# Performance work log

Hardware: AMD Instinct MI355X
Metric: run time of the kernel (lower is better)

The kernel has to match this reference:

```python
import jax, jax.numpy as jnp
import numpy as np

DIM = 2048
H = 16
HD = DIM // H          # 128
ROPE_CH = (HD // 2) // 2 * 2  # 64
EPS = 1e-6
SCALE = HD ** -0.5
MAX_WAVELENGTH = 10000.0


def rmsnorm(v, w):
    vf = v.astype(jnp.float32)
    var = jnp.mean(vf * vf, axis=-1, keepdims=True)
    return (w * (vf * jax.lax.rsqrt(var + EPS))).astype(v.dtype)


def apply_rope(v, pos):
    # v: [B, S, H, C], pos: [B, S]
    C = v.shape[-1]
    frac = 2.0 * jnp.arange(C // 2, dtype=jnp.float32) / C
    timescale = MAX_WAVELENGTH ** frac                      # [C/2]
    ang = pos[:, :, None].astype(jnp.float32) / timescale   # [B, S, C/2]
    ang = ang[:, :, None, :]                                 # [B, S, 1, C/2]
    sin, cos = jnp.sin(ang), jnp.cos(ang)
    v1, v2 = jnp.split(v, 2, axis=-1)
    return jnp.concatenate([v1 * cos - v2 * sin, v2 * cos + v1 * sin], axis=-1).astype(v.dtype)


def apply_rotary_emb(v, pos, channels):
    # rope only the last `channels` of head_dim
    left, right = v[..., :-channels], v[..., -channels:]
    return jnp.concatenate([left, apply_rope(right, pos)], axis=-1)


def project_qkv(t, W, b, qn, kn):
    B, N, _ = t.shape
    qkv = t @ W + b                                          # [B, N, 3*H*HD]
    q, k, v = jnp.split(qkv, [H * HD, 2 * H * HD], axis=-1)
    q = rmsnorm(q.reshape(B, N, H, HD), qn)
    k = rmsnorm(k.reshape(B, N, H, HD), kn)
    v = v.reshape(B, N, H, HD)
    return q, k, v


def setup_inputs() -> dict:
    key = jax.random.key(0)
    ks = jax.random.split(key, 12)
    B, NX, NY = 2, 2048, 512
    x = jax.random.normal(ks[0], (B, NX, DIM), dtype=jnp.float32)
    y = jax.random.normal(ks[1], (B, NY, DIM), dtype=jnp.float32)
    temporal_pos = jax.random.randint(ks[2], (B, NX), 0, 2048)
    y_temporal_pos = jax.random.randint(ks[3], (B, NY), 0, 512)
    s = 0.02
    Wqkv_x = jax.random.normal(ks[4], (DIM, 3 * H * HD), dtype=jnp.float32) * s
    bqkv_x = jnp.zeros((3 * H * HD,), dtype=jnp.float32)
    Wqkv_y = jax.random.normal(ks[5], (DIM, 3 * H * HD), dtype=jnp.float32) * s
    bqkv_y = jnp.zeros((3 * H * HD,), dtype=jnp.float32)
    Wproj_x = jax.random.normal(ks[6], (DIM, DIM), dtype=jnp.float32) * s
    bproj_x = jnp.zeros((DIM,), dtype=jnp.float32)
    Wproj_y = jax.random.normal(ks[7], (DIM, DIM), dtype=jnp.float32) * s
    bproj_y = jnp.zeros((DIM,), dtype=jnp.float32)
    qnx = jnp.ones((HD,), dtype=jnp.float32)
    knx = jnp.ones((HD,), dtype=jnp.float32)
    qny = jnp.ones((HD,), dtype=jnp.float32)
    kny = jnp.ones((HD,), dtype=jnp.float32)
    return {"x": x, "y": y, "temporal_pos": temporal_pos, "y_temporal_pos": y_temporal_pos,
            "Wqkv_x": Wqkv_x, "bqkv_x": bqkv_x, "qnx": qnx, "knx": knx,
            "Wproj_x": Wproj_x, "bproj_x": bproj_x,
            "Wqkv_y": Wqkv_y, "bqkv_y": bqkv_y, "qny": qny, "kny": kny,
            "Wproj_y": Wproj_y, "bproj_y": bproj_y}


def reference(x, y, temporal_pos, y_temporal_pos,
              Wqkv_x, bqkv_x, qnx, knx, Wproj_x, bproj_x,
              Wqkv_y, bqkv_y, qny, kny, Wproj_y, bproj_y):
    B, NX, _ = x.shape
    NY = y.shape[1]
    qx, kx, vx = project_qkv(x, Wqkv_x, bqkv_x, qnx, knx)   # [B, NX, H, HD]
    qy, ky, vy = project_qkv(y, Wqkv_y, bqkv_y, qny, kny)   # [B, NY, H, HD]
    # RoPE on last ROPE_CH channels of head_dim (rope_dim=-1)
    qx = apply_rotary_emb(qx, temporal_pos, ROPE_CH)
    kx = apply_rotary_emb(kx, temporal_pos, ROPE_CH)
    qy = apply_rotary_emb(qy, y_temporal_pos, ROPE_CH)
    ky = apply_rotary_emb(ky, y_temporal_pos, ROPE_CH)
    # joint attention over concatenated x/y tokens
    q = jnp.concatenate([qx, qy], axis=1)   # [B, S, H, HD]
    k = jnp.concatenate([kx, ky], axis=1)
    v = jnp.concatenate([vx, vy], axis=1)
    scores = jnp.einsum('bqhd,bkhd->bhqk', q, k) * SCALE
    attn = jax.nn.softmax(scores, axis=-1)
    out = jnp.einsum('bhqk,bkhd->bqhd', attn, v)             # [B, S, H, HD]
    out = out.reshape(B, NX + NY, DIM).astype(x.dtype)
    x_out = out[:, :NX] @ Wproj_x + bproj_x
    y_out = out[:, NX:] @ Wproj_y + bproj_y
    return (x_out, y_out)
```

## Files before the change

### kernel.cpp

```cpp
#include <hip/hip_runtime.h>
#include <stdint.h>

typedef __attribute__((ext_vector_type(8))) short v8s;
typedef __attribute__((ext_vector_type(4))) float v4f;

#define DEV static __device__ __forceinline__

DEV unsigned short f2bf(float f) {
  union { float f; unsigned int u; } v; v.f = f;
  unsigned int u = v.u;
  return (unsigned short)((u + 0x7fffu + ((u >> 16) & 1u)) >> 16);
}

DEV v4f mfma16(v8s a, v8s b, v4f c) {
  return __builtin_amdgcn_mfma_f32_16x16x32_bf16(a, b, c, 0, 0, 0);
}

DEV unsigned int cvtpk(float lo, float hi) {
  unsigned int r;
  asm("v_cvt_pk_bf16_f32 %0, %1, %2" : "=v"(r) : "v"(lo), "v"(hi));
  return r;
}

DEV void async16(const void* g, void* lds) {
  __builtin_amdgcn_global_load_lds((const __attribute__((address_space(1))) unsigned int*)g,
                                   (__attribute__((address_space(3))) unsigned int*)lds,
                                   16, 0, 0);
}

__global__ __launch_bounds__(256) void k_f32_to_bf16(const float* __restrict__ in,
                                                     unsigned short* __restrict__ out, int n4) {
  int i = blockIdx.x * 256 + threadIdx.x;
  if (i < n4) {
    float4 v = reinterpret_cast<const float4*>(in)[i];
    ushort4 o;
    o.x = f2bf(v.x); o.y = f2bf(v.y); o.z = f2bf(v.z); o.w = f2bf(v.w);
    reinterpret_cast<ushort4*>(out)[i] = o;
  }
}

__global__ __launch_bounds__(256) void k_rope_tbl(const int* __restrict__ pos,
                                                  float* __restrict__ tbl, int nrows) {
  int idx = blockIdx.x * 256 + threadIdx.x;
  if (idx < nrows * 32) {
    int row = idx >> 5, i = idx & 31;
    float ang = (float)pos[row] * expf((float)i * -0.2878231366f);
    float sv, cv;
    sincosf(ang, &sv, &cv);
    reinterpret_cast<float2*>(tbl)[(size_t)row * 32 + i] = make_float2(cv, sv);
  }
}

__global__ __launch_bounds__(256) void k_transpose(const float* __restrict__ in,
                                                   unsigned short* __restrict__ out, int R, int C) {
  __shared__ float tile[64][65];
  const int r0 = blockIdx.x * 64, c0 = blockIdx.y * 64;
  const int t = threadIdx.x;
  const int rl = t >> 4, cl = (t & 15) * 4;
#pragma unroll
  for (int p = 0; p < 4; p++) {
    const int r = rl + p * 16;
    float4 v = *reinterpret_cast<const float4*>(&in[(size_t)(r0 + r) * C + c0 + cl]);
    tile[r][cl] = v.x; tile[r][cl + 1] = v.y; tile[r][cl + 2] = v.z; tile[r][cl + 3] = v.w;
  }
  __syncthreads();
  const int cw = t >> 4, rw = (t & 15) * 4;
#pragma unroll
  for (int p = 0; p < 4; p++) {
    const int c = cw + p * 16;
    ushort4 o;
    o.x = f2bf(tile[rw + 0][c]); o.y = f2bf(tile[rw + 1][c]);
    o.z = f2bf(tile[rw + 2][c]); o.w = f2bf(tile[rw + 3][c]);
    *reinterpret_cast<ushort4*>(&out[(size_t)(c0 + c) * R + r0 + rw]) = o;
  }
}

template <int MODE>
__global__ __launch_bounds__(256) void k_gemm(
    const unsigned short* __restrict__ A, const unsigned short* __restrict__ Bt,
    const float* __restrict__ bias, float* __restrict__ Cout,
    unsigned short* __restrict__ Qb, unsigned short* __restrict__ Kb,
    unsigned short* __restrict__ Vt, const float* __restrict__ qn,
    const float* __restrict__ kn, const float* __restrict__ rtbl, int K, int N, int Nm, int noff,
    int rows_per_b, int b_stride, int row_off) {
  __shared__ __align__(16) char Lds[3 * 16384];
  __shared__ float red[4][64];
  const int m0 = blockIdx.x * 128, n0 = blockIdx.y * 128;
  const int t = threadIdx.x, l = t & 63, w = t >> 6;
  const int lg = l >> 4, li = l & 15;
  const int sr = t >> 2, ss = t & 3;

  auto amap = [&](int m) -> size_t {
    return (size_t)(m / rows_per_b) * b_stride + row_off + (m % rows_per_b);
  };
  const int ssw = (ss ^ ((sr >> 1) & 3)) * 8;
  const unsigned short* ap0 = A + amap(m0 + sr) * K + ssw;
  const unsigned short* ap1 = A + amap(m0 + sr + 64) * K + ssw;
  const unsigned short* bp0 = Bt + (size_t)(n0 + sr) * K + ssw;
  const unsigned short* bp1 = bp0 + (size_t)64 * K;

  auto stage = [&](char* lb, int st) {
    const int ko = st * 32;
    async16(ap0 + ko, lb + w * 1024);
    async16(ap1 + ko, lb + w * 1024 + 4096);
    async16(bp0 + ko, lb + 8192 + w * 1024);
    async16(bp1 + ko, lb + 8192 + w * 1024 + 4096);
  };

  int aoff[4], boff[4];
#pragma unroll
  for (int mf = 0; mf < 4; mf++) {
    const int row = (w >> 1) * 64 + mf * 16 + li;
    aoff[mf] = row * 64 + ((lg ^ ((row >> 1) & 3)) * 16);
  }
#pragma unroll
  for (int nf = 0; nf < 4; nf++) {
    const int row = (w & 1) * 64 + nf * 16 + li;
    boff[nf] = 8192 + row * 64 + ((lg ^ ((row >> 1) & 3)) * 16);
  }

  v4f acc[4][4] = {};
  const int NK = K >> 5;

  stage(Lds, 0);
  stage(Lds + 16384, 1);
  stage(Lds + 32768, 2);

  int bufc = 0;
  for (int tt = 0; tt < NK; tt++) {
    asm volatile("s_waitcnt vmcnt(8)" ::: "memory");
    __builtin_amdgcn_sched_barrier(0);
    __builtin_amdgcn_s_barrier();
    __builtin_amdgcn_sched_barrier(0);
    char* Bf = Lds + bufc;
    v8s af[4], bf[4];
#pragma unroll
    for (int mf = 0; mf < 4; mf++) af[mf] = *reinterpret_cast<const v8s*>(Bf + aoff[mf]);
#pragma unroll
    for (int nf = 0; nf < 4; nf++) bf[nf] = *reinterpret_cast<const v8s*>(Bf + boff[nf]);
    __builtin_amdgcn_s_setprio(1);
#pragma unroll
    for (int mf = 0; mf < 4; mf++)
#pragma unroll
      for (int nf = 0; nf < 4; nf++)
        acc[mf][nf] = mfma16(af[mf], bf[nf], acc[mf][nf]);
    __builtin_amdgcn_s_setprio(0);
    __builtin_amdgcn_sched_barrier(0);
    __builtin_amdgcn_s_barrier();
    __builtin_amdgcn_sched_barrier(0);
    const int st = (tt + 3 < NK) ? tt + 3 : NK - 1;
    stage(Bf, st);
    bufc += 16384;
    if (bufc == 49152) bufc = 0;
  }
  asm volatile("s_waitcnt vmcnt(0)" ::: "memory");

  const int colh = (w & 1) * 64;
#pragma unroll
  for (int nf = 0; nf < 4; nf++) {
    const float bv = bias[n0 + colh + nf * 16 + li];
#pragma unroll
    for (int mf = 0; mf < 4; mf++)
#pragma unroll
      for (int r = 0; r < 4; r++) acc[mf][nf][r] += bv;
  }

  if (MODE == 0) {
#pragma unroll
    for (int mf = 0; mf < 4; mf++) {
      const int row = m0 + (w >> 1) * 64 + mf * 16 + lg * 4;
#pragma unroll
      for (int nf = 0; nf < 4; nf++) {
        const int col = n0 + colh + nf * 16 + li;
#pragma unroll
        for (int r = 0; r < 4; r++) Cout[(size_t)(row + r) * N + col] = acc[mf][nf][r];
      }
    }
    return;
  }

  const int sec = n0 >> 11;
  const int h = (n0 >> 7) & 15;
  const int mrow0 = m0 + (w >> 1) * 64;

  if (sec < 2) {
    float ss_[4][4];
#pragma unroll
    for (int mf = 0; mf < 4; mf++)
#pragma unroll
      for (int r = 0; r < 4; r++) {
        float s = 0.f;
#pragma unroll
        for (int nf = 0; nf < 4; nf++) s += acc[mf][nf][r] * acc[mf][nf][r];
#pragma unroll
        for (int off = 1; off < 16; off <<= 1) s += __shfl_xor(s, off, 64);
        ss_[mf][r] = s;
      }
    if (li == 0) {
#pragma unroll
      for (int mf = 0; mf < 4; mf++)
#pragma unroll
        for (int r = 0; r < 4; r++) red[w][mf * 16 + lg * 4 + r] = ss_[mf][r];
    }
    __syncthreads();
    const float* gw = (sec == 0) ? qn : kn;
    unsigned short* Out = (sec == 0) ? Qb : Kb;
    float g[4];
#pragma unroll
    for (int nf = 0; nf < 4; nf++) g[nf] = gw[colh + nf * 16 + li];
#pragma unroll
    for (int mf = 0; mf < 4; mf++) {
#pragma unroll
      for (int r = 0; r < 4; r++) {
        const int m = mrow0 + mf * 16 + lg * 4 + r;
        const float tot = ss_[mf][r] + red[w ^ 1][mf * 16 + lg * 4 + r];
        const float rn = rsqrtf(tot * (1.0f / 128.0f) + 1e-6f);
        float vv[4];
#pragma unroll
        for (int nf = 0; nf < 4; nf++) vv[nf] = acc[mf][nf][r] * rn * g[nf];
        if (colh) {
#pragma unroll
          for (int nf = 0; nf < 2; nf++) {
            const float2 cs = reinterpret_cast<const float2*>(rtbl)[(size_t)m * 32 + nf * 16 + li];
            const float v1 = vv[nf], v2 = vv[nf + 2];
            vv[nf] = v1 * cs.x - v2 * cs.y;
            vv[nf + 2] = v2 * cs.x + v1 * cs.y;
          }
        }
        const int b = m / Nm, n = m - b * Nm;
        const size_t base = ((size_t)(b * 16 + h) * 2560 + noff + n) * 128 + colh;
#pragma unroll
        for (int nf = 0; nf < 4; nf++) Out[base + nf * 16 + li] = f2bf(vv[nf]);
      }
    }
  } else {
#pragma unroll
    for (int mf = 0; mf < 4; mf++) {
      const int m = mrow0 + mf * 16 + lg * 4;
      const int b = m / Nm, n = m - b * Nm;
      const int key = noff + n;
      const size_t base = ((size_t)(b * 16 + h) * 80 + (key >> 5)) * 4096 + (key & 31);
#pragma unroll
      for (int nf = 0; nf < 4; nf++) {
        const int chan = colh + nf * 16 + li;
        ushort4 o;
        o.x = f2bf(acc[mf][nf][0]); o.y = f2bf(acc[mf][nf][1]);
        o.z = f2bf(acc[mf][nf][2]); o.w = f2bf(acc[mf][nf][3]);
        *reinterpret_cast<ushort4*>(&Vt[base + chan * 32]) = o;
      }
    }
  }
}

__global__ __launch_bounds__(256) void k_attn(const unsigned short* __restrict__ Qb,
                                              const unsigned short* __restrict__ Kb,
                                              const unsigned short* __restrict__ Vt,
                                              unsigned short* __restrict__ Ob) {
  __shared__ __align__(16) char Ldss[3 * 16384];
  const int NT = 2560;
  const float SC = 0.08838834764831845f;
  const float FM = 12.0f;
  const int i = blockIdx.x;
  const int xcd = i & 7, j = i >> 3;
  const int qt = j % 20;
  const int bh = xcd * 4 + j / 20;
  const int b = bh >> 4, h = bh & 15;
  const int t = threadIdx.x, l = t & 63, w = t >> 6;
  const int lg = l >> 4, li = l & 15;
  const unsigned short* Qbase = Qb + ((size_t)bh * NT + qt * 128) * 128;
  const unsigned short* Kbase = Kb + (size_t)bh * NT * 128;
  const unsigned short* Vbase = Vt + (size_t)bh * 327680;

  v8s qf[2][4];
#pragma unroll
  for (int mg = 0; mg < 2; mg++) {
    const int row = w * 32 + mg * 16 + li;
#pragma unroll
    for (int ds = 0; ds < 4; ds++)
      qf[mg][ds] = *reinterpret_cast<const v8s*>(Qbase + (size_t)row * 128 + (lg + ds * 4) * 8);
  }

  auto stage = [&](char* lb, int st) {
#pragma unroll
    for (int p = 0; p < 2; p++) {
      const int rho = w * 4 + (l >> 4) + p * 16;
      const int key = ((rho >> 2) & 3) * 8 + ((rho >> 4) & 1) * 4 + (rho & 3);
      const char* g = (const char*)Kbase + ((size_t)(st * 32 + key)) * 256 +
                      (((l & 15) ^ (rho & 7)) * 16);
      async16(g, lb + w * 1024 + p * 4096);
    }
#pragma unroll
    for (int p = 0; p < 2; p++) {
      const int d = w * 32 + p * 16 + (l >> 2);
      const char* g = (const char*)Vbase + (size_t)st * 8192 + d * 64 +
                      ((((l & 3) * 2) ^ (d & 6)) * 8);
      async16(g, lb + 8192 + w * 2048 + p * 1024);
    }
  };

  int koff[2][4], voff[8];
#pragma unroll
  for (int kf = 0; kf < 2; kf++)
#pragma unroll
    for (int ds = 0; ds < 4; ds++) {
      const int row = kf * 16 + li;
      koff[kf][ds] = row * 256 + (((lg + ds * 4) ^ (row & 7)) * 16);
    }
#pragma unroll
  for (int df = 0; df < 8; df++) {
    const int d = df * 16 + li;
    voff[df] = 8192 + d * 64 + (((lg * 2) ^ (d & 6)) * 8);
  }

  float ps[2] = {0.f, 0.f};
  v4f O_[2][8] = {};

  stage(Ldss, 0);
  stage(Ldss + 16384, 1);
  stage(Ldss + 32768, 2);

  int bufc = 0;
  for (int tt = 0; tt < 80; tt++) {
    asm volatile("s_waitcnt vmcnt(8)" ::: "memory");
    __builtin_amdgcn_sched_barrier(0);
    __builtin_amdgcn_s_barrier();
    __builtin_amdgcn_sched_barrier(0);
    char* B = Ldss + bufc;

    v4f s[2][2] = {};
    __builtin_amdgcn_s_setprio(1);
#pragma unroll
    for (int kf = 0; kf < 2; kf++)
#pragma unroll
      for (int ds = 0; ds < 4; ds++) {
        v8s ka = *reinterpret_cast<const v8s*>(B + koff[kf][ds]);
        s[0][kf] = mfma16(ka, qf[0][ds], s[0][kf]);
        s[1][kf] = mfma16(ka, qf[1][ds], s[1][kf]);
      }
    __builtin_amdgcn_s_setprio(0);

    v8s pa[2];
#pragma unroll
    for (int mg = 0; mg < 2; mg++) {
      float p[2][4];
#pragma unroll
      for (int kf = 0; kf < 2; kf++)
#pragma unroll
        for (int r = 0; r < 4; r++) {
          p[kf][r] = __expf(fmaf(s[mg][kf][r], SC, -FM));
          ps[mg] += p[kf][r];
        }
      union { v8s v; unsigned int u[4]; } pk;
      pk.u[0] = cvtpk(p[0][0], p[0][1]);
      pk.u[1] = cvtpk(p[0][2], p[0][3]);
      pk.u[2] = cvtpk(p[1][0], p[1][1]);
      pk.u[3] = cvtpk(p[1][2], p[1][3]);
      pa[mg] = pk.v;
    }

    __builtin_amdgcn_s_setprio(1);
#pragma unroll
    for (int df = 0; df < 8; df++) {
      v8s vb = *reinterpret_cast<const v8s*>(B + voff[df]);
      O_[0][df] = mfma16(pa[0], vb, O_[0][df]);
      O_[1][df] = mfma16(pa[1], vb, O_[1][df]);
    }
    __builtin_amdgcn_s_setprio(0);

    __builtin_amdgcn_sched_barrier(0);
    __builtin_amdgcn_s_barrier();
    __builtin_amdgcn_sched_barrier(0);
    const int st = (tt + 3 < 80) ? tt + 3 : 79;
    stage(B, st);
    bufc += 16384;
    if (bufc == 49152) bufc = 0;
  }
  asm volatile("s_waitcnt vmcnt(0)" ::: "memory");

#pragma unroll
  for (int mg = 0; mg < 2; mg++) {
    ps[mg] += __shfl_xor(ps[mg], 16, 64);
    ps[mg] += __shfl_xor(ps[mg], 32, 64);
  }
#pragma unroll
  for (int mg = 0; mg < 2; mg++) {
    float inv[4];
#pragma unroll
    for (int r = 0; r < 4; r++) inv[r] = 1.0f / __shfl(ps[mg], lg * 4 + r, 64);
#pragma unroll
    for (int df = 0; df < 8; df++) {
      const int d = df * 16 + li;
#pragma unroll
      for (int r = 0; r < 4; r++) {
        const int q = qt * 128 + w * 32 + mg * 16 + lg * 4 + r;
        Ob[((size_t)b * NT + q) * 2048 + h * 128 + d] = f2bf(O_[mg][df][r] * inv[r]);
      }
    }
  }
}

extern "C" void kernel_launch(void* const* d_in, const int* in_sizes, int n_in,
                              void* d_out, int out_size, void* d_ws, size_t ws_size,
                              hipStream_t stream) {
  (void)in_sizes; (void)n_in; (void)out_size;
  const float* x = (const float*)d_in[0];
  const float* y = (const float*)d_in[1];
  const int* tpos = (const int*)d_in[2];
  const int* ypos = (const int*)d_in[3];
  const float* Wqkv_x = (const float*)d_in[4];
  const float* bqkv_x = (const float*)d_in[5];
  const float* qnx = (const float*)d_in[6];
  const float* knx = (const float*)d_in[7];
  const float* Wproj_x = (const float*)d_in[8];
  const float* bproj_x = (const float*)d_in[9];
  const float* Wqkv_y = (const float*)d_in[10];
  const float* bqkv_y = (const float*)d_in[11];
  const float* qny = (const float*)d_in[12];
  const float* kny = (const float*)d_in[13];
  const float* Wproj_y = (const float*)d_in[14];
  const float* bproj_y = (const float*)d_in[15];
  float* outp = (float*)d_out;

  char* ws = (char*)d_ws;
  size_t off = 0;
  auto alloc = [&](size_t b) {
    char* p = ws + off;
    off += (b + 255) & ~(size_t)255;
    return p;
  };
  unsigned short* Wt = (unsigned short*)alloc(6144ull * 2048 * 2);
  unsigned short* xb = (unsigned short*)alloc(4096ull * 2048 * 2);
  unsigned short* yb = (unsigned short*)alloc(1024ull * 2048 * 2);
  unsigned short* Qbf = (unsigned short*)alloc(2ull * 16 * 2560 * 128 * 2);
  unsigned short* Kbf = (unsigned short*)alloc(2ull * 16 * 2560 * 128 * 2);
  unsigned short* Vtb = (unsigned short*)alloc(2ull * 16 * 80 * 128 * 32 * 2);
  unsigned short* Obf = (unsigned short*)alloc(2ull * 2560 * 2048 * 2);
  float* rtx = (float*)alloc(4096ull * 64 * 4);
  float* rty = (float*)alloc(1024ull * 64 * 4);
  if (ws_size < off) return;

  k_f32_to_bf16<<<8192, 256, 0, stream>>>(x, xb, 2097152);
  k_f32_to_bf16<<<2048, 256, 0, stream>>>(y, yb, 524288);
  k_rope_tbl<<<512, 256, 0, stream>>>(tpos, rtx, 4096);
  k_rope_tbl<<<128, 256, 0, stream>>>(ypos, rty, 1024);

  k_transpose<<<dim3(32, 96), 256, 0, stream>>>(Wqkv_x, Wt, 2048, 6144);
  k_gemm<1><<<dim3(32, 48), 256, 0, stream>>>(xb, Wt, bqkv_x, nullptr, Qbf, Kbf, Vtb, qnx, knx,
                                              rtx, 2048, 6144, 2048, 0, 4096, 0, 0);
  k_transpose<<<dim3(32, 96), 256, 0, stream>>>(Wqkv_y, Wt, 2048, 6144);
  k_gemm<1><<<dim3(8, 48), 256, 0, stream>>>(yb, Wt, bqkv_y, nullptr, Qbf, Kbf, Vtb, qny, kny,
                                             rty, 2048, 6144, 512, 2048, 1024, 0, 0);

  k_attn<<<640, 256, 0, stream>>>(Qbf, Kbf, Vtb, Obf);

  k_transpose<<<dim3(32, 32), 256, 0, stream>>>(Wproj_x, Wt, 2048, 2048);
  k_gemm<0><<<dim3(32, 16), 256, 0, stream>>>(Obf, Wt, bproj_x, outp, nullptr, nullptr, nullptr,
                                              nullptr, nullptr, nullptr, 2048, 2048, 0, 0, 2048,
                                              2560, 0);
  k_transpose<<<dim3(32, 32), 256, 0, stream>>>(Wproj_y, Wt, 2048, 2048);
  k_gemm<0><<<dim3(8, 16), 256, 0, stream>>>(Obf, Wt, bproj_y, outp + 8388608ull, nullptr, nullptr,
                                             nullptr, nullptr, nullptr, nullptr, 2048, 2048, 0, 0,
                                             512, 2560, 2048);
}
```

Baseline: 486.3 us.

## Retile GEMM to 128x256 blocks with 8 waves and XCD-aware block ordering

The GEMM now runs 512-thread blocks on 128x256 output tiles. Each wave covers 32 rows by a full 128-column head, so the RMSNorm reduction stays inside one wave and the LDS cross-wave reduction and __syncthreads are gone. The grid is flattened and remapped so consecutive blocks on each XCD share tiles for better L2 reuse. The risks are higher LDS use per block, fewer A-fragment reuses per B load, and lower occupancy on the small y launches.

```diff
diff --git a/kernel.cpp b/kernel.cpp
--- a/kernel.cpp
+++ b/kernel.cpp
@@ -76,102 +76,99 @@
 }
 
 template <int MODE>
-__global__ __launch_bounds__(256) void k_gemm(
+__global__ __launch_bounds__(512, 4) void k_gemm(
     const unsigned short* __restrict__ A, const unsigned short* __restrict__ Bt,
     const float* __restrict__ bias, float* __restrict__ Cout,
     unsigned short* __restrict__ Qb, unsigned short* __restrict__ Kb,
     unsigned short* __restrict__ Vt, const float* __restrict__ qn,
     const float* __restrict__ kn, const float* __restrict__ rtbl, int K, int N, int Nm, int noff,
-    int rows_per_b, int b_stride, int row_off) {
-  __shared__ __align__(16) char Lds[3 * 16384];
-  __shared__ float red[4][64];
-  const int m0 = blockIdx.x * 128, n0 = blockIdx.y * 128;
+    int rows_per_b, int b_stride, int row_off, int Mb) {
+  __shared__ __align__(16) char Lds[3 * 24576];
+  const int chunk = gridDim.x >> 3;
+  const int o = (blockIdx.x & 7) * chunk + (blockIdx.x >> 3);
+  const int m0 = (o % Mb) * 128, n0 = (o / Mb) * 256;
   const int t = threadIdx.x, l = t & 63, w = t >> 6;
   const int lg = l >> 4, li = l & 15;
-  const int sr = t >> 2, ss = t & 3;
+  const int wr = w >> 1, wc = w & 1;
 
   auto amap = [&](int m) -> size_t {
     return (size_t)(m / rows_per_b) * b_stride + row_off + (m % rows_per_b);
   };
-  const int ssw = (ss ^ ((sr >> 1) & 3)) * 8;
-  const unsigned short* ap0 = A + amap(m0 + sr) * K + ssw;
-  const unsigned short* ap1 = A + amap(m0 + sr + 64) * K + ssw;
-  const unsigned short* bp0 = Bt + (size_t)(n0 + sr) * K + ssw;
-  const unsigned short* bp1 = bp0 + (size_t)64 * K;
+  const int ar = t >> 2, as = t & 3;
+  const int asw = (as ^ ((ar >> 1) & 3)) * 8;
+  const unsigned short* ap = A + amap(m0 + ar) * K + asw;
+  const unsigned short* bp0 = Bt + (size_t)(n0 + ar) * K + asw;
+  const unsigned short* bp1 = bp0 + (size_t)128 * K;
+  const int t16 = t * 16;
 
   auto stage = [&](char* lb, int st) {
     const int ko = st * 32;
-    async16(ap0 + ko, lb + w * 1024);
-    async16(ap1 + ko, lb + w * 1024 + 4096);
-    async16(bp0 + ko, lb + 8192 + w * 1024);
-    async16(bp1 + ko, lb + 8192 + w * 1024 + 4096);
+    async16(ap + ko, lb + t16);
+    async16(bp0 + ko, lb + 8192 + t16);
+    async16(bp1 + ko, lb + 16384 + t16);
   };
 
-  int aoff[4], boff[4];
-#pragma unroll
-  for (int mf = 0; mf < 4; mf++) {
-    const int row = (w >> 1) * 64 + mf * 16 + li;
+  int aoff[2], boff[8];
+#pragma unroll
+  for (int mf = 0; mf < 2; mf++) {
+    const int row = wr * 32 + mf * 16 + li;
     aoff[mf] = row * 64 + ((lg ^ ((row >> 1) & 3)) * 16);
   }
 #pragma unroll
-  for (int nf = 0; nf < 4; nf++) {
-    const int row = (w & 1) * 64 + nf * 16 + li;
+  for (int nf = 0; nf < 8; nf++) {
+    const int row = wc * 128 + nf * 16 + li;
     boff[nf] = 8192 + row * 64 + ((lg ^ ((row >> 1) & 3)) * 16);
   }
 
-  v4f acc[4][4] = {};
+  v4f acc[2][8] = {};
   const int NK = K >> 5;
 
   stage(Lds, 0);
-  stage(Lds + 16384, 1);
-  stage(Lds + 32768, 2);
+  stage(Lds + 24576, 1);
+  stage(Lds + 49152, 2);
 
   int bufc = 0;
   for (int tt = 0; tt < NK; tt++) {
-    asm volatile("s_waitcnt vmcnt(8)" ::: "memory");
+    asm volatile("s_waitcnt vmcnt(6)" ::: "memory");
     __builtin_amdgcn_sched_barrier(0);
     __builtin_amdgcn_s_barrier();
     __builtin_amdgcn_sched_barrier(0);
     char* Bf = Lds + bufc;
-    v8s af[4], bf[4];
-#pragma unroll
-    for (int mf = 0; mf < 4; mf++) af[mf] = *reinterpret_cast<const v8s*>(Bf + aoff[mf]);
-#pragma unroll
-    for (int nf = 0; nf < 4; nf++) bf[nf] = *reinterpret_cast<const v8s*>(Bf + boff[nf]);
+    v8s af0 = *reinterpret_cast<const v8s*>(Bf + aoff[0]);
+    v8s af1 = *reinterpret_cast<const v8s*>(Bf + aoff[1]);
     __builtin_amdgcn_s_setprio(1);
 #pragma unroll
-    for (int mf = 0; mf < 4; mf++)
-#pragma unroll
-      for (int nf = 0; nf < 4; nf++)
-        acc[mf][nf] = mfma16(af[mf], bf[nf], acc[mf][nf]);
+    for (int nf = 0; nf < 8; nf++) {
+      v8s bfv = *reinterpret_cast<const v8s*>(Bf + boff[nf]);
+      acc[0][nf] = mfma16(af0, bfv, acc[0][nf]);
+      acc[1][nf] = mfma16(af1, bfv, acc[1][nf]);
+    }
     __builtin_amdgcn_s_setprio(0);
     __builtin_amdgcn_sched_barrier(0);
     __builtin_amdgcn_s_barrier();
     __builtin_amdgcn_sched_barrier(0);
-    const int st = (tt + 3 < NK) ? tt + 3 : NK - 1;
-    stage(Bf, st);
-    bufc += 16384;
-    if (bufc == 49152) bufc = 0;
+    stage(Bf, (tt + 3 < NK) ? tt + 3 : NK - 1);
+    bufc += 24576;
+    if (bufc == 73728) bufc = 0;
   }
   asm volatile("s_waitcnt vmcnt(0)" ::: "memory");
 
-  const int colh = (w & 1) * 64;
-#pragma unroll
-  for (int nf = 0; nf < 4; nf++) {
-    const float bv = bias[n0 + colh + nf * 16 + li];
-#pragma unroll
-    for (int mf = 0; mf < 4; mf++)
+#pragma unroll
+  for (int nf = 0; nf < 8; nf++) {
+    const float bv = bias[n0 + wc * 128 + nf * 16 + li];
+#pragma unroll
+    for (int mf = 0; mf < 2; mf++)
 #pragma unroll
       for (int r = 0; r < 4; r++) acc[mf][nf][r] += bv;
   }
 
   if (MODE == 0) {
 #pragma unroll
-    for (int mf = 0; mf < 4; mf++) {
-      const int row = m0 + (w >> 1) * 64 + mf * 16 + lg * 4;
-#pragma unroll
-      for (int nf = 0; nf < 4; nf++) {
-        const int col = n0 + colh + nf * 16 + li;
+    for (int mf = 0; mf < 2; mf++) {
+      const int row = m0 + wr * 32 + mf * 16 + lg * 4;
+#pragma unroll
+      for (int nf = 0; nf < 8; nf++) {
+        const int col = n0 + wc * 128 + nf * 16 + li;
 #pragma unroll
         for (int r = 0; r < 4; r++) Cout[(size_t)(row + r) * N + col] = acc[mf][nf][r];
       }
@@ -180,73 +177,57 @@
   }
 
   const int sec = n0 >> 11;
-  const int h = (n0 >> 7) & 15;
-  const int mrow0 = m0 + (w >> 1) * 64;
+  const int hh = ((n0 + wc * 128) >> 7) & 15;
+  const int mrow0 = m0 + wr * 32;
 
   if (sec < 2) {
-    float ss_[4][4];
-#pragma unroll
-    for (int mf = 0; mf < 4; mf++)
+    const float* gw = (sec == 0) ? qn : kn;
+    unsigned short* Out = (sec == 0) ? Qb : Kb;
+    float g[8];
+#pragma unroll
+    for (int nf = 0; nf < 8; nf++) g[nf] = gw[nf * 16 + li];
+#pragma unroll
+    for (int mf = 0; mf < 2; mf++) {
 #pragma unroll
       for (int r = 0; r < 4; r++) {
         float s = 0.f;
 #pragma unroll
-        for (int nf = 0; nf < 4; nf++) s += acc[mf][nf][r] * acc[mf][nf][r];
+        for (int nf = 0; nf < 8; nf++) s += acc[mf][nf][r] * acc[mf][nf][r];
 #pragma unroll
         for (int off = 1; off < 16; off <<= 1) s += __shfl_xor(s, off, 64);
-        ss_[mf][r] = s;
-      }
-    if (li == 0) {
-#pragma unroll
-      for (int mf = 0; mf < 4; mf++)
-#pragma unroll
-        for (int r = 0; r < 4; r++) red[w][mf * 16 + lg * 4 + r] = ss_[mf][r];
-    }
-    __syncthreads();
-    const float* gw = (sec == 0) ? qn : kn;
-    unsigned short* Out = (sec == 0) ? Qb : Kb;
-    float g[4];
-#pragma unroll
-    for (int nf = 0; nf < 4; nf++) g[nf] = gw[colh + nf * 16 + li];
-#pragma unroll
-    for (int mf = 0; mf < 4; mf++) {
-#pragma unroll
-      for (int r = 0; r < 4; r++) {
         const int m = mrow0 + mf * 16 + lg * 4 + r;
-        const float tot = ss_[mf][r] + red[w ^ 1][mf * 16 + lg * 4 + r];
-        const float rn = rsqrtf(tot * (1.0f / 128.0f) + 1e-6f);
-        float vv[4];
-#pragma unroll
-        for (int nf = 0; nf < 4; nf++) vv[nf] = acc[mf][nf][r] * rn * g[nf];
-        if (colh) {
-#pragma unroll
-          for (int nf = 0; nf < 2; nf++) {
-            const float2 cs = reinterpret_cast<const float2*>(rtbl)[(size_t)m * 32 + nf * 16 + li];
-            const float v1 = vv[nf], v2 = vv[nf + 2];
-            vv[nf] = v1 * cs.x - v2 * cs.y;
-            vv[nf + 2] = v2 * cs.x + v1 * cs.y;
-          }
+        const float rn = rsqrtf(s * (1.0f / 128.0f) + 1e-6f);
+        float vv[8];
+#pragma unroll
+        for (int nf = 0; nf < 8; nf++) vv[nf] = acc[mf][nf][r] * rn * g[nf];
+#pragma unroll
+        for (int nf = 4; nf < 6; nf++) {
+          const float2 cs =
+              reinterpret_cast<const float2*>(rtbl)[(size_t)m * 32 + (nf - 4) * 16 + li];
+          const float v1 = vv[nf], v2 = vv[nf + 2];
+          vv[nf] = v1 * cs.x - v2 * cs.y;
+          vv[nf + 2] = v2 * cs.x + v1 * cs.y;
         }
         const int b = m / Nm, n = m - b * Nm;
-        const size_t base = ((size_t)(b * 16 + h) * 2560 + noff + n) * 128 + colh;
-#pragma unroll
-        for (int nf = 0; nf < 4; nf++) Out[base + nf * 16 + li] = f2bf(vv[nf]);
+        const size_t base = ((size_t)(b * 16 + hh) * 2560 + noff + n) * 128;
+#pragma unroll
+        for (int nf = 0; nf < 8; nf++) Out[base + nf * 16 + li] = f2bf(vv[nf]);
       }
     }
   } else {
 #pragma unroll
-    for (int mf = 0; mf < 4; mf++) {
+    for (int mf = 0; mf < 2; mf++) {
       const int m = mrow0 + mf * 16 + lg * 4;
       const int b = m / Nm, n = m - b * Nm;
       const int key = noff + n;
-      const size_t base = ((size_t)(b * 16 + h) * 80 + (key >> 5)) * 4096 + (key & 31);
-#pragma unroll
-      for (int nf = 0; nf < 4; nf++) {
-        const int chan = colh + nf * 16 + li;
-        ushort4 o;
-        o.x = f2bf(acc[mf][nf][0]); o.y = f2bf(acc[mf][nf][1]);
-        o.z = f2bf(acc[mf][nf][2]); o.w = f2bf(acc[mf][nf][3]);
-        *reinterpret_cast<ushort4*>(&Vt[base + chan * 32]) = o;
+      const size_t base = ((size_t)(b * 16 + hh) * 80 + (key >> 5)) * 4096 + (key & 31);
+#pragma unroll
+      for (int nf = 0; nf < 8; nf++) {
+        const int chan = nf * 16 + li;
+        ushort4 ov;
+        ov.x = f2bf(acc[mf][nf][0]); ov.y = f2bf(acc[mf][nf][1]);
+        ov.z = f2bf(acc[mf][nf][2]); ov.w = f2bf(acc[mf][nf][3]);
+        *reinterpret_cast<ushort4*>(&Vt[base + chan * 32]) = ov;
       }
     }
   }
@@ -445,20 +426,19 @@
   k_rope_tbl<<<128, 256, 0, stream>>>(ypos, rty, 1024);
 
   k_transpose<<<dim3(32, 96), 256, 0, stream>>>(Wqkv_x, Wt, 2048, 6144);
-  k_gemm<1><<<dim3(32, 48), 256, 0, stream>>>(xb, Wt, bqkv_x, nullptr, Qbf, Kbf, Vtb, qnx, knx,
-                                              rtx, 2048, 6144, 2048, 0, 4096, 0, 0);
+  k_gemm<1><<<768, 512, 0, stream>>>(xb, Wt, bqkv_x, nullptr, Qbf, Kbf, Vtb, qnx, knx, rtx, 2048,
+                                     6144, 2048, 0, 4096, 0, 0, 32);
   k_transpose<<<dim3(32, 96), 256, 0, stream>>>(Wqkv_y, Wt, 2048, 6144);
-  k_gemm<1><<<dim3(8, 48), 256, 0, stream>>>(yb, Wt, bqkv_y, nullptr, Qbf, Kbf, Vtb, qny, kny,
-                                             rty, 2048, 6144, 512, 2048, 1024, 0, 0);
+  k_gemm<1><<<192, 512, 0, stream>>>(yb, Wt, bqkv_y, nullptr, Qbf, Kbf, Vtb, qny, kny, rty, 2048,
+                                     6144, 512, 2048, 1024, 0, 0, 8);
 
   k_attn<<<640, 256, 0, stream>>>(Qbf, Kbf, Vtb, Obf);
 
   k_transpose<<<dim3(32, 32), 256, 0, stream>>>(Wproj_x, Wt, 2048, 2048);
-  k_gemm<0><<<dim3(32, 16), 256, 0, stream>>>(Obf, Wt, bproj_x, outp, nullptr, nullptr, nullptr,
-                                              nullptr, nullptr, nullptr, 2048, 2048, 0, 0, 2048,
-                                              2560, 0);
+  k_gemm<0><<<256, 512, 0, stream>>>(Obf, Wt, bproj_x, outp, nullptr, nullptr, nullptr, nullptr,
+                                     nullptr, nullptr, 2048, 2048, 0, 0, 2048, 2560, 0, 32);
   k_transpose<<<dim3(32, 32), 256, 0, stream>>>(Wproj_y, Wt, 2048, 2048);
-  k_gemm<0><<<dim3(8, 16), 256, 0, stream>>>(Obf, Wt, bproj_y, outp + 8388608ull, nullptr, nullptr,
-                                             nullptr, nullptr, nullptr, nullptr, 2048, 2048, 0, 0,
-                                             512, 2560, 2048);
-}
+  k_gemm<0><<<64, 512, 0, stream>>>(Obf, Wt, bproj_y, outp + 8388608ull, nullptr, nullptr, nullptr,
+                                    nullptr, nullptr, nullptr, 2048, 2048, 0, 0, 512, 2560, 2048,
+                                    8);
+}
```

Result: faster. 444.2 us (-8.7%).
